# Kernel tuning notes

Measured on AMD Instinct MI355X. Metric: run time of the kernel, lower is better.

## Reference

```python
import jax, jax.numpy as jnp
import numpy as np

N_ATOM, N_CHI, N_BOND, N_DIR = 119, 3, 5, 3
NUM_LAYER, EMB, FEAT, NG = 5, 300, 256, 4096
N_NODES, N_EDGES = 100000, 200000


def setup_inputs() -> dict:
    key = jax.random.key(0)
    ks = jax.random.split(key, 16)
    N, E = N_NODES, N_EDGES
    r = lambda k, s, sc: jax.random.normal(k, s, jnp.float32) * sc
    inp = {}
    inp["atom_type"] = jax.random.randint(ks[0], (N,), 0, N_ATOM, dtype=jnp.int32)
    inp["chirality"] = jax.random.randint(ks[1], (N,), 0, N_CHI, dtype=jnp.int32)
    inp["edge_index"] = jax.random.randint(ks[2], (2, E), 0, N, dtype=jnp.int32)
    inp["edge_type"] = jax.random.randint(ks[3], (E,), 0, 4, dtype=jnp.int32)
    inp["edge_dir"] = jax.random.randint(ks[4], (E,), 0, N_DIR, dtype=jnp.int32)
    inp["batch"] = jnp.sort(jax.random.randint(ks[5], (N,), 0, NG, dtype=jnp.int32))
    inp["atom_emb1"] = r(ks[6], (N_ATOM, EMB), 0.02)
    inp["atom_emb2"] = r(ks[7], (N_CHI, EMB), 0.02)
    inp["W"] = r(ks[8], (NUM_LAYER, EMB, EMB), 0.05)
    inp["b"] = jnp.zeros((NUM_LAYER, EMB), jnp.float32)
    inp["ee1"] = r(ks[9], (NUM_LAYER, N_BOND, 1), 0.5)
    inp["ee2"] = r(ks[10], (NUM_LAYER, N_DIR, 1), 0.5)
    inp["bn_gamma"] = jnp.ones((NUM_LAYER, EMB), jnp.float32)
    inp["bn_beta"] = jnp.zeros((NUM_LAYER, EMB), jnp.float32)
    inp["feat_W"] = r(ks[11], (EMB, FEAT), 0.05)
    inp["feat_b"] = jnp.zeros((FEAT,), jnp.float32)
    inp["head_W1"] = r(ks[12], (FEAT, FEAT // 2), 0.08)
    inp["head_b1"] = jnp.zeros((FEAT // 2,), jnp.float32)
    inp["head_W2"] = r(ks[13], (FEAT // 2, 2), 0.1)
    inp["head_b2"] = jnp.zeros((2,), jnp.float32)
    return inp


def reference(atom_type, chirality, edge_index, edge_type, edge_dir, batch,
              atom_emb1, atom_emb2, W, b, ee1, ee2, bn_gamma, bn_beta,
              feat_W, feat_b, head_W1, head_b1, head_W2, head_b2):
    N = atom_type.shape[0]
    # add self loops (edge_attr: bond_type=4, direction=0)
    loops = jnp.arange(N, dtype=edge_index.dtype)
    row = jnp.concatenate([edge_index[0], loops])
    col = jnp.concatenate([edge_index[1], loops])
    et = jnp.concatenate([edge_type, jnp.full((N,), 4, edge_type.dtype)])
    ed = jnp.concatenate([edge_dir, jnp.zeros((N,), edge_dir.dtype)])

    h = atom_emb1[atom_type] + atom_emb2[chirality]  # [N, EMB]
    for l in range(NUM_LAYER):
        hx = h @ W[l]                                  # [N, EMB]
        edge_emb = ee1[l][et] + ee2[l][ed]             # [E+N, 1]
        msg = hx[row] + edge_emb                       # gather + broadcast add
        out = jax.ops.segment_sum(msg, col, num_segments=N) + b[l]
        # BatchNorm1d (training-mode batch stats, eps=1e-5)
        mean = out.mean(axis=0)
        var = out.var(axis=0)
        h = bn_gamma[l] * (out - mean) * jax.lax.rsqrt(var + 1e-5) + bn_beta[l]
        if l < NUM_LAYER - 1:
            h = jax.nn.relu(h)  # drop_ratio=0 -> dropout is identity

    # global mean pool over graphs
    sums = jax.ops.segment_sum(h, batch, num_segments=NG)              # [NG, EMB]
    counts = jax.ops.segment_sum(jnp.ones((N, 1), h.dtype), batch, num_segments=NG)
    hg = sums / jnp.maximum(counts, 1.0)

    hf = hg @ feat_W + feat_b                                          # [NG, FEAT]
    pred = jax.nn.softplus(hf @ head_W1 + head_b1) @ head_W2 + head_b2  # [NG, 2]
    return hf, pred
```

## Files before the change

### kernel.cpp

```cpp
#include <hip/hip_runtime.h>
#include <math.h>

typedef unsigned short u16;
typedef unsigned int u32;
typedef short v8s __attribute__((ext_vector_type(8)));
typedef float v4f __attribute__((ext_vector_type(4)));

#define EMB 300
#define SP 320
#define NGRP 4096
#define FEAT 256
#define MT 128
#define NT 160
#define NCOMB 357
#define NREP 32

__device__ __forceinline__ u16 f2bf(float x) {
    u32 u = __float_as_uint(x);
    u += 0x7FFFu + ((u >> 16) & 1u);
    return (u16)(u >> 16);
}
__device__ __forceinline__ float bf2f(u16 h) {
    return __uint_as_float((u32)h << 16);
}
__device__ __forceinline__ void unpack8(uint4 w, float* o) {
    const u32* p = &w.x;
#pragma unroll
    for (int q = 0; q < 4; q++) {
        o[2 * q]     = __uint_as_float(p[q] << 16);
        o[2 * q + 1] = __uint_as_float(p[q] & 0xFFFF0000u);
    }
}
__device__ __forceinline__ v8s clampA(uint4 w, float4 ta, float4 tb) {
    const u32* p = &w.x;
    float t[8] = {ta.x, ta.y, ta.z, ta.w, tb.x, tb.y, tb.z, tb.w};
    u32 o[4];
#pragma unroll
    for (int q = 0; q < 4; q++) {
        float lo = __uint_as_float(p[q] << 16);
        float hi = __uint_as_float(p[q] & 0xFFFF0000u);
        lo = fmaxf(lo, t[2 * q]);
        hi = fmaxf(hi, t[2 * q + 1]);
        o[q] = (__float_as_uint(lo) >> 16) | (__float_as_uint(hi) & 0xFFFF0000u);
    }
    uint4 r = make_uint4(o[0], o[1], o[2], o[3]);
    return *(v8s*)&r;
}
__device__ __forceinline__ void dma16(const u16* g, u16* l) {
    __builtin_amdgcn_global_load_lds(
        (const __attribute__((address_space(1))) unsigned int*)g,
        (__attribute__((address_space(3))) unsigned int*)l, 16, 0, 0);
}

__global__ void k_prep_n(const int* __restrict__ at, const int* __restrict__ ch,
                         int* __restrict__ c9, int* __restrict__ deg,
                         int* __restrict__ cursor, int N) {
    int n = blockIdx.x * blockDim.x + threadIdx.x;
    if (n < N) {
        c9[n] = at[n] * 3 + ch[n];
        deg[n] = 0;
        cursor[n] = 0;
    }
}

__global__ void k_count(const int* __restrict__ col, int* __restrict__ deg, int E) {
    int e = blockIdx.x * blockDim.x + threadIdx.x;
    if (e < E) atomicAdd(&deg[col[e]], 1);
}

__global__ __launch_bounds__(256) void k_bsum(const int* __restrict__ deg,
                                              int* __restrict__ bsum, int N) {
    int base = blockIdx.x * 1024 + threadIdx.x * 4;
    int s = 0;
    if (base + 3 < N) {
        int4 v = *(const int4*)(deg + base);
        s = v.x + v.y + v.z + v.w;
    } else {
        for (int j = 0; j < 4; j++) if (base + j < N) s += deg[base + j];
    }
    __shared__ int red[256];
    red[threadIdx.x] = s;
    __syncthreads();
    for (int off = 128; off > 0; off >>= 1) {
        if (threadIdx.x < off) red[threadIdx.x] += red[threadIdx.x + off];
        __syncthreads();
    }
    if (threadIdx.x == 0) bsum[blockIdx.x] = red[0];
}

__global__ __launch_bounds__(128) void k_scanb(const int* __restrict__ bsum,
                                               int* __restrict__ boff, int NB) {
    __shared__ int sh[128];
    int t = threadIdx.x;
    int v = (t < NB) ? bsum[t] : 0;
    sh[t] = v;
    __syncthreads();
    for (int off = 1; off < 128; off <<= 1) {
        int add = (t >= off) ? sh[t - off] : 0;
        __syncthreads();
        sh[t] += add;
        __syncthreads();
    }
    if (t < NB) boff[t] = sh[t] - v;
}

__global__ __launch_bounds__(256) void k_indptr(const int* __restrict__ deg,
                                                const int* __restrict__ boff,
                                                int* __restrict__ indptr, int N) {
    int b = blockIdx.x, t = threadIdx.x;
    int base = b * 1024 + t * 4;
    int v[4] = {0, 0, 0, 0};
    if (base + 3 < N) {
        int4 w = *(const int4*)(deg + base);
        v[0] = w.x; v[1] = w.y; v[2] = w.z; v[3] = w.w;
    } else {
        for (int j = 0; j < 4; j++) if (base + j < N) v[j] = deg[base + j];
    }
    int tsum = v[0] + v[1] + v[2] + v[3];
    __shared__ int sh[256];
    sh[t] = tsum;
    __syncthreads();
    for (int off = 1; off < 256; off <<= 1) {
        int add = (t >= off) ? sh[t - off] : 0;
        __syncthreads();
        sh[t] += add;
        __syncthreads();
    }
    int run = boff[b] + sh[t] - tsum;
    for (int j = 0; j < 4; j++) {
        run += v[j];
        if (base + j < N) indptr[base + j + 1] = run;
    }
    if (b == 0 && t == 0) indptr[0] = 0;
}

__global__ void k_fill(const int* __restrict__ row, const int* __restrict__ col,
                       const int* __restrict__ et, const int* __restrict__ ed,
                       const int* __restrict__ indptr, int* __restrict__ cursor,
                       int* __restrict__ packed, int E) {
    int e = blockIdx.x * blockDim.x + threadIdx.x;
    if (e >= E) return;
    int c = col[e];
    int pos = indptr[c] + atomicAdd(&cursor[c], 1);
    packed[pos] = row[e] | ((et[e] * 3 + ed[e]) << 17);
}

__global__ void k_comb(const float* __restrict__ e1, const float* __restrict__ e2,
                       u16* __restrict__ comb) {
    int idx = blockIdx.x * blockDim.x + threadIdx.x;
    if (idx >= NCOMB * 40) return;
    int row = idx / 40, f = idx % 40;
    int at = row / 3, ch = row % 3;
    u32 o[4];
#pragma unroll
    for (int q = 0; q < 4; q++) {
        int c0 = f * 8 + q * 2;
        float x0 = 0.f, x1 = 0.f;
        if (c0 < EMB)     x0 = e1[(size_t)at * EMB + c0] + e2[(size_t)ch * EMB + c0];
        if (c0 + 1 < EMB) x1 = e1[(size_t)at * EMB + c0 + 1] + e2[(size_t)ch * EMB + c0 + 1];
        o[q] = (u32)f2bf(x0) | ((u32)f2bf(x1) << 16);
    }
    *(uint4*)(comb + (size_t)row * SP + f * 8) = make_uint4(o[0], o[1], o[2], o[3]);
}

__global__ __launch_bounds__(320) void k_wprep(
    const float* __restrict__ Wl, const float* __restrict__ sc,
    const float* __restrict__ sh, u16* __restrict__ Wt, float* __restrict__ srow) {
    __shared__ float wred[5];
    int n = blockIdx.x;
    int k = threadIdx.x;
    float w = 0.f;
    if (n < EMB && k < EMB) w = Wl[(size_t)k * EMB + n];
    Wt[(size_t)n * SP + k] = f2bf(w * sc[k]);
    float s = (k < EMB) ? sh[k] * w : 0.f;
#pragma unroll
    for (int o2 = 32; o2 > 0; o2 >>= 1) s += __shfl_down(s, o2);
    if ((k & 63) == 0) wred[k >> 6] = s;
    __syncthreads();
    if (k == 0) {
        float t = wred[0] + wred[1] + wred[2] + wred[3] + wred[4];
        srow[n] = (n < EMB) ? t : 0.f;
    }
}

__global__ void k_ident(float* __restrict__ sc, float* __restrict__ sh,
                        float* __restrict__ thr, float* __restrict__ colstats) {
    int c = threadIdx.x;
    if (c < SP) {
        sc[c] = (c < EMB) ? 1.f : 0.f;
        sh[c] = 0.f;
        thr[c] = -__builtin_inff();
        for (int r = 0; r < NREP; r++) {
            colstats[r * 2 * SP + c] = 0.f;
            colstats[r * 2 * SP + SP + c] = 0.f;
        }
    }
}

__global__ void k_finalize(float* __restrict__ cs,
                           const float* __restrict__ gamma, const float* __restrict__ beta,
                           float* __restrict__ sc, float* __restrict__ sh,
                           float* __restrict__ thr, int N) {
    int c = threadIdx.x;
    if (c >= SP) return;
    float s1 = 0.f, s2 = 0.f;
    for (int r = 0; r < NREP; r++) {
        s1 += cs[r * 2 * SP + c];
        s2 += cs[r * 2 * SP + SP + c];
        cs[r * 2 * SP + c] = 0.f;
        cs[r * 2 * SP + SP + c] = 0.f;
    }
    if (c < EMB) {
        float inv = 1.f / (float)N;
        float mean = s1 * inv;
        float var = s2 * inv - mean * mean;
        float rstd = rsqrtf(fmaxf(var, 0.f) + 1e-5f);
        float s = gamma[c] * rstd;
        float b = beta[c] - mean * s;
        sc[c] = s;
        sh[c] = b;
        thr[c] = bf2f(f2bf(-b / s));
    } else {
        sc[c] = 0.f; sh[c] = 0.f; thr[c] = -__builtin_inff();
    }
}

__global__ __launch_bounds__(256) void k_gemm(
    const u16* __restrict__ A, const u16* __restrict__ Wt,
    const float* __restrict__ thr, const float* __restrict__ srow,
    u16* __restrict__ C, int M, const int* __restrict__ rowmap) {
    __shared__ __align__(16) u16 sm[21504];

    int m0 = blockIdx.y * MT;
    int n0 = blockIdx.x * NT;
    int tid = threadIdx.x;
    int wave = tid >> 6, lane = tid & 63;
    int wm = wave >> 1, wn = wave & 1;
    int lm = lane & 15, quad = lane >> 4;

    int ar0 = min(m0 + (tid >> 2), M - 1);
    int ar1 = min(m0 + 64 + (tid >> 2), M - 1);
    if (rowmap) { ar0 = rowmap[ar0]; ar1 = rowmap[ar1]; }
    const u16* ag0 = A + (size_t)ar0 * SP + (tid & 3) * 8;
    const u16* ag1 = A + (size_t)ar1 * SP + (tid & 3) * 8;
    const u16* bg0 = Wt + (size_t)(n0 + (tid >> 2)) * SP + (tid & 3) * 8;
    const u16* bg1 = Wt + (size_t)(n0 + 64 + (tid >> 2)) * SP + (tid & 3) * 8;
    const u16* bg2 = Wt + (size_t)(n0 + 128 + (tid >> 2)) * SP + (tid & 3) * 8;

    const float* tp = thr + quad * 8;

    v4f acc[4][5];
#pragma unroll
    for (int nf = 0; nf < 5; nf++) {
        float sv = srow[n0 + wn * 80 + nf * 16 + lm];
#pragma unroll
        for (int mf = 0; mf < 4; mf++)
            acc[mf][nf] = (v4f){sv, sv, sv, sv};
    }

    auto issue = [&](int d, int kt) {
        int ko = kt * 32;
        u16* ad = sm + d * 4096;
        u16* bd = sm + 8192 + d * 5120;
        dma16(ag0 + ko, ad + tid * 8);
        dma16(ag1 + ko, ad + (256 + tid) * 8);
        dma16(bg0 + ko, bd + tid * 8);
        dma16(bg1 + ko, bd + (256 + tid) * 8);
        if (tid < 128) dma16(bg2 + ko, bd + (512 + tid) * 8);
    };

    issue(0, 0);
    for (int kt = 0; kt < SP / 32; kt++) {
        __syncthreads();
        if (kt + 1 < SP / 32) issue((kt + 1) & 1, kt + 1);
        const u16* as = sm + (kt & 1) * 4096;
        const u16* bs = sm + 8192 + (kt & 1) * 5120;
        float4 ta = *(const float4*)(tp + kt * 32);
        float4 tb = *(const float4*)(tp + kt * 32 + 4);
        v8s b[5], a[4];
#pragma unroll
        for (int nf = 0; nf < 5; nf++)
            b[nf] = *(const v8s*)(bs + (wn * 80 + nf * 16 + lm) * 32 + quad * 8);
#pragma unroll
        for (int mf = 0; mf < 4; mf++) {
            uint4 w = *(const uint4*)(as + (wm * 64 + mf * 16 + lm) * 32 + quad * 8);
            a[mf] = clampA(w, ta, tb);
        }
#pragma unroll
        for (int nf = 0; nf < 5; nf++)
#pragma unroll
            for (int mf = 0; mf < 4; mf++)
                acc[mf][nf] = __builtin_amdgcn_mfma_f32_16x16x32_bf16(a[mf], b[nf], acc[mf][nf], 0, 0, 0);
    }

    __syncthreads();
#pragma unroll
    for (int mf = 0; mf < 4; mf++)
#pragma unroll
        for (int nf = 0; nf < 5; nf++)
#pragma unroll
            for (int r = 0; r < 4; r++)
                sm[(wm * 64 + mf * 16 + quad * 4 + r) * 168 + wn * 80 + nf * 16 + lm] =
                    f2bf(acc[mf][nf][r]);
    __syncthreads();
#pragma unroll
    for (int i = 0; i < 10; i++) {
        int slot = tid + i * 256;
        int r = slot / 20, cg = slot % 20;
        if (m0 + r < M)
            *(uint4*)(C + (size_t)(m0 + r) * SP + n0 + cg * 8) =
                *(const uint4*)(sm + r * 168 + cg * 8);
    }
}

__global__ __launch_bounds__(320) void k_aggf(
    const u16* __restrict__ Q, const int* __restrict__ indptr,
    const int* __restrict__ packed, const float* __restrict__ e1,
    const float* __restrict__ e2, u16* __restrict__ P,
    float* __restrict__ colstats, int N) {
    __shared__ float tab[15];
    __shared__ float part[8][328];
    int tid = threadIdx.x;
    if (tid < 15) tab[tid] = e1[tid / 3] + e2[tid % 3];
    __syncthreads();
    int f = tid % 40;
    int slot = tid / 40;
    int n = blockIdx.x * 8 + slot;

    float psum[8] = {0, 0, 0, 0, 0, 0, 0, 0};
    float psq[8]  = {0, 0, 0, 0, 0, 0, 0, 0};

    if (n < N) {
        float acc[8];
        unpack8(*(const uint4*)(Q + (size_t)n * SP + f * 8), acc);
        float s = tab[12];
        int i = indptr[n], e = indptr[n + 1];
        int pk = (i < e) ? packed[i] : 0;
        while (i < e) {
            uint4 g = *(const uint4*)(Q + (size_t)(pk & 0x1FFFF) * SP + f * 8);
            int nx = i + 1;
            int pkn = (nx < e) ? packed[nx] : 0;
            float t[8];
            unpack8(g, t);
#pragma unroll
            for (int q = 0; q < 8; q++) acc[q] += t[q];
            s += tab[pk >> 17];
            i = nx; pk = pkn;
        }
        u32 o[4];
#pragma unroll
        for (int q = 0; q < 4; q++) {
            float r0 = acc[2 * q] + s;
            float r1 = acc[2 * q + 1] + s;
            psum[2 * q] = r0;      psum[2 * q + 1] = r1;
            psq[2 * q]  = r0 * r0; psq[2 * q + 1]  = r1 * r1;
            o[q] = (u32)f2bf(r0) | ((u32)f2bf(r1) << 16);
        }
        *(uint4*)(P + (size_t)n * SP + f * 8) = make_uint4(o[0], o[1], o[2], o[3]);
    }

    int rep = (blockIdx.x & (NREP - 1)) * 2 * SP;
#pragma unroll
    for (int j = 0; j < 8; j++) part[slot][f * 8 + j] = psum[j];
    __syncthreads();
    {
        float s = 0.f;
#pragma unroll
        for (int k = 0; k < 8; k++) s += part[k][tid];
        atomicAdd(&colstats[rep + tid], s);
    }
    __syncthreads();
#pragma unroll
    for (int j = 0; j < 8; j++) part[slot][f * 8 + j] = psq[j];
    __syncthreads();
    {
        float s = 0.f;
#pragma unroll
        for (int k = 0; k < 8; k++) s += part[k][tid];
        atomicAdd(&colstats[rep + SP + tid], s);
    }
}

__global__ void k_bounds(const int* __restrict__ batch, int* __restrict__ gstart, int N) {
    int n = blockIdx.x * blockDim.x + threadIdx.x;
    if (n > N) return;
    int bcur = (n < N) ? batch[n] : NGRP;
    int bprev = (n > 0) ? batch[n - 1] : -1;
    for (int g = bprev + 1; g <= bcur; g++) gstart[g] = n;
}

__global__ __launch_bounds__(320) void k_pool(
    const u16* __restrict__ P, const float* __restrict__ sc,
    const float* __restrict__ sh, const int* __restrict__ gstart,
    float* __restrict__ hg) {
    int tid = threadIdx.x;
    int g = blockIdx.x * 8 + tid / 40;
    int f = tid % 40;
    int r0 = gstart[g], r1 = gstart[g + 1];
    int cnt = r1 - r0;
    float acc[8] = {0, 0, 0, 0, 0, 0, 0, 0};
    for (int r = r0; r < r1; r++) {
        float t[8];
        unpack8(*(const uint4*)(P + (size_t)r * SP + f * 8), t);
#pragma unroll
        for (int j = 0; j < 8; j++) acc[j] += t[j];
    }
    float inv = 1.f / (float)max(cnt, 1);
#pragma unroll
    for (int j = 0; j < 8; j++) {
        int c = f * 8 + j;
        if (c < EMB)
            hg[(size_t)g * EMB + c] = (acc[j] * sc[c] + (float)cnt * sh[c]) * inv;
    }
}

__global__ __launch_bounds__(256) void k_feat(const float* __restrict__ hg,
                                              const float* __restrict__ fW,
                                              const float* __restrict__ fb,
                                              float* __restrict__ hf) {
    __shared__ float hgs[16 * EMB];
    int g0 = blockIdx.x * 16;
    int tid = threadIdx.x;
    for (int i = tid; i < 16 * EMB; i += 256) {
        int gi = i / EMB, c = i % EMB;
        hgs[i] = hg[(size_t)(g0 + gi) * EMB + c];
    }
    __syncthreads();
    float acc[16];
    float fbv = fb[tid];
#pragma unroll
    for (int gi = 0; gi < 16; gi++) acc[gi] = fbv;
    for (int k = 0; k < EMB; k++) {
        float w = fW[(size_t)k * FEAT + tid];
#pragma unroll
        for (int gi = 0; gi < 16; gi++) acc[gi] += hgs[gi * EMB + k] * w;
    }
#pragma unroll
    for (int gi = 0; gi < 16; gi++) hf[(size_t)(g0 + gi) * FEAT + tid] = acc[gi];
}

__global__ __launch_bounds__(128) void k_head(const float* __restrict__ hf,
                                              const float* __restrict__ W1,
                                              const float* __restrict__ b1,
                                              const float* __restrict__ W2,
                                              const float* __restrict__ b2,
                                              float* __restrict__ pred) {
    __shared__ float hfs[8 * FEAT];
    __shared__ float sred[2][8][2];
    int g0 = blockIdx.x * 8;
    int tid = threadIdx.x;
    for (int i = tid; i < 8 * FEAT; i += 128) {
        int gi = i >> 8, k = i & 255;
        hfs[i] = hf[(size_t)(g0 + gi) * FEAT + k];
    }
    __syncthreads();
    float acc[8];
    float b1v = b1[tid];
#pragma unroll
    for (int gi = 0; gi < 8; gi++) acc[gi] = b1v;
    for (int k = 0; k < FEAT; k++) {
        float w = W1[(size_t)k * 128 + tid];
#pragma unroll
        for (int gi = 0; gi < 8; gi++) acc[gi] += hfs[gi * FEAT + k] * w;
    }
    float w20 = W2[tid * 2], w21 = W2[tid * 2 + 1];
    int wv = tid >> 6;
#pragma unroll
    for (int gi = 0; gi < 8; gi++) {
        float x = acc[gi];
        float t = fmaxf(x, 0.f) + log1pf(expf(-fabsf(x)));
        float p0 = t * w20, p1 = t * w21;
#pragma unroll
        for (int off = 32; off > 0; off >>= 1) {
            p0 += __shfl_down(p0, off);
            p1 += __shfl_down(p1, off);
        }
        if ((tid & 63) == 0) { sred[wv][gi][0] = p0; sred[wv][gi][1] = p1; }
    }
    __syncthreads();
    if (tid < 16) {
        int gi = tid >> 1, o = tid & 1;
        pred[(size_t)(g0 + gi) * 2 + o] = sred[0][gi][o] + sred[1][gi][o] + b2[o];
    }
}

extern "C" void kernel_launch(void* const* d_in, const int* in_sizes, int n_in,
                              void* d_out, int out_size, void* d_ws, size_t ws_size,
                              hipStream_t stream) {
    const int* atom_type = (const int*)d_in[0];
    const int* chir      = (const int*)d_in[1];
    const int* eidx      = (const int*)d_in[2];
    const int* etype     = (const int*)d_in[3];
    const int* edir      = (const int*)d_in[4];
    const int* batch     = (const int*)d_in[5];
    const float* emb1    = (const float*)d_in[6];
    const float* emb2    = (const float*)d_in[7];
    const float* W       = (const float*)d_in[8];
    const float* ee1     = (const float*)d_in[10];
    const float* ee2     = (const float*)d_in[11];
    const float* gamma   = (const float*)d_in[12];
    const float* beta    = (const float*)d_in[13];
    const float* featW   = (const float*)d_in[14];
    const float* featb   = (const float*)d_in[15];
    const float* hW1     = (const float*)d_in[16];
    const float* hb1     = (const float*)d_in[17];
    const float* hW2     = (const float*)d_in[18];
    const float* hb2     = (const float*)d_in[19];

    int N = in_sizes[0];
    int E = in_sizes[2] / 2;
    const int* erow = eidx;
    const int* ecol = eidx + E;

    size_t off = 0;
    char* base = (char*)d_ws;
    auto carve = [&](size_t bytes) -> void* {
        void* p = base + off;
        off += (bytes + 255) & ~(size_t)255;
        return p;
    };
    u16*   P        = (u16*)  carve((size_t)N * SP * 2);
    u16*   Q        = (u16*)  carve((size_t)N * SP * 2);
    u16*   Wt       = (u16*)  carve((size_t)SP * SP * 2);
    u16*   comb     = (u16*)  carve((size_t)NCOMB * SP * 2);
    int*   c9map    = (int*)  carve((size_t)N * 4);
    int*   deg      = (int*)  carve((size_t)N * 4);
    int*   cursor   = (int*)  carve((size_t)N * 4);
    int*   indptr   = (int*)  carve((size_t)(N + 1) * 4);
    int*   packed   = (int*)  carve((size_t)E * 4);
    int*   bsum     = (int*)  carve(1024 * 4);
    int*   boff     = (int*)  carve(1024 * 4);
    float* colstats = (float*)carve((size_t)NREP * 2 * SP * 4);
    float* scale_id = (float*)carve(SP * 4);
    float* shift_id = (float*)carve(SP * 4);
    float* thr_id   = (float*)carve(SP * 4);
    float* scale_bn = (float*)carve(SP * 4);
    float* shift_bn = (float*)carve(SP * 4);
    float* thr_bn   = (float*)carve(SP * 4);
    float* srow     = (float*)carve(SP * 4);
    int*   gstart   = (int*)  carve((size_t)(NGRP + 1) * 4);
    float* hg       = (float*)carve((size_t)NGRP * EMB * 4);

    float* hf   = (float*)d_out;
    float* pred = (float*)d_out + (size_t)NGRP * FEAT;

    int eb = (E + 255) / 256;
    int NB = (N + 1023) / 1024;
    k_prep_n<<<(N + 255) / 256, 256, 0, stream>>>(atom_type, chir, c9map, deg, cursor, N);
    k_count<<<eb, 256, 0, stream>>>(ecol, deg, E);
    k_bsum<<<NB, 256, 0, stream>>>(deg, bsum, N);
    k_scanb<<<1, 128, 0, stream>>>(bsum, boff, NB);
    k_indptr<<<NB, 256, 0, stream>>>(deg, boff, indptr, N);
    k_fill<<<eb, 256, 0, stream>>>(erow, ecol, etype, edir, indptr, cursor, packed, E);

    k_comb<<<(NCOMB * 40 + 255) / 256, 256, 0, stream>>>(emb1, emb2, comb);
    k_ident<<<1, SP, 0, stream>>>(scale_id, shift_id, thr_id, colstats);

    const float* sc = scale_id;
    const float* sh = shift_id;
    const float* th = thr_id;
    dim3 ggrid(2, (N + MT - 1) / MT);
    int ab = (N + 7) / 8;
    for (int l = 0; l < 5; l++) {
        k_wprep<<<SP, 320, 0, stream>>>(W + (size_t)l * EMB * EMB, sc, sh, Wt, srow);
        if (l == 0)
            k_gemm<<<ggrid, 256, 0, stream>>>(comb, Wt, th, srow, Q, N, c9map);
        else
            k_gemm<<<ggrid, 256, 0, stream>>>(P, Wt, th, srow, Q, N, nullptr);
        k_aggf<<<ab, 320, 0, stream>>>(Q, indptr, packed, ee1 + l * 5, ee2 + l * 3, P,
                                       colstats, N);
        k_finalize<<<1, SP, 0, stream>>>(colstats, gamma + l * EMB, beta + l * EMB,
                                         scale_bn, shift_bn, thr_bn, N);
        sc = scale_bn; sh = shift_bn; th = thr_bn;
    }

    k_bounds<<<(N + 1 + 255) / 256, 256, 0, stream>>>(batch, gstart, N);
    k_pool<<<NGRP / 8, 320, 0, stream>>>(P, scale_bn, shift_bn, gstart, hg);
    k_feat<<<NGRP / 16, 256, 0, stream>>>(hg, featW, featb, hf);
    k_head<<<NGRP / 8, 128, 0, stream>>>(hf, hW1, hb1, hW2, hb2, pred);
}
```

Measured before the change: 718.9 us.

## Load GEMM B operand directly from global and halve shared memory footprint

The GEMM kernel stops staging the weight (B) tiles through LDS and has each lane read its B fragment straight from global memory, relying on cache since the weights are small and reused across blocks. The epilogue writes the output tile through LDS in two halves so the shared buffer can shrink to half its former size. The intent is to cut LDS traffic and footprint so more blocks can be resident per CU. In exchange, B reads become per-lane global loads with 16-byte strided access inside the inner loop, which adds latency and an extra barrier in the epilogue.

```diff
diff --git a/kernel.cpp b/kernel.cpp
--- a/kernel.cpp
+++ b/kernel.cpp
@@ -229,7 +229,7 @@
     const u16* __restrict__ A, const u16* __restrict__ Wt,
     const float* __restrict__ thr, const float* __restrict__ srow,
     u16* __restrict__ C, int M, const int* __restrict__ rowmap) {
-    __shared__ __align__(16) u16 sm[21504];
+    __shared__ __align__(16) u16 sm[10752];
 
     int m0 = blockIdx.y * MT;
     int n0 = blockIdx.x * NT;
@@ -243,9 +243,7 @@
     if (rowmap) { ar0 = rowmap[ar0]; ar1 = rowmap[ar1]; }
     const u16* ag0 = A + (size_t)ar0 * SP + (tid & 3) * 8;
     const u16* ag1 = A + (size_t)ar1 * SP + (tid & 3) * 8;
-    const u16* bg0 = Wt + (size_t)(n0 + (tid >> 2)) * SP + (tid & 3) * 8;
-    const u16* bg1 = Wt + (size_t)(n0 + 64 + (tid >> 2)) * SP + (tid & 3) * 8;
-    const u16* bg2 = Wt + (size_t)(n0 + 128 + (tid >> 2)) * SP + (tid & 3) * 8;
+    const u16* bp = Wt + (size_t)(n0 + wn * 80 + lm) * SP + quad * 8;
 
     const float* tp = thr + quad * 8;
 
@@ -261,12 +259,8 @@
     auto issue = [&](int d, int kt) {
         int ko = kt * 32;
         u16* ad = sm + d * 4096;
-        u16* bd = sm + 8192 + d * 5120;
         dma16(ag0 + ko, ad + tid * 8);
         dma16(ag1 + ko, ad + (256 + tid) * 8);
-        dma16(bg0 + ko, bd + tid * 8);
-        dma16(bg1 + ko, bd + (256 + tid) * 8);
-        if (tid < 128) dma16(bg2 + ko, bd + (512 + tid) * 8);
     };
 
     issue(0, 0);
@@ -274,13 +268,12 @@
         __syncthreads();
         if (kt + 1 < SP / 32) issue((kt + 1) & 1, kt + 1);
         const u16* as = sm + (kt & 1) * 4096;
-        const u16* bs = sm + 8192 + (kt & 1) * 5120;
         float4 ta = *(const float4*)(tp + kt * 32);
         float4 tb = *(const float4*)(tp + kt * 32 + 4);
         v8s b[5], a[4];
 #pragma unroll
         for (int nf = 0; nf < 5; nf++)
-            b[nf] = *(const v8s*)(bs + (wn * 80 + nf * 16 + lm) * 32 + quad * 8);
+            b[nf] = *(const v8s*)(bp + (size_t)nf * 16 * SP + kt * 32);
 #pragma unroll
         for (int mf = 0; mf < 4; mf++) {
             uint4 w = *(const uint4*)(as + (wm * 64 + mf * 16 + lm) * 32 + quad * 8);
@@ -295,21 +288,28 @@
 
     __syncthreads();
 #pragma unroll
-    for (int mf = 0; mf < 4; mf++)
-#pragma unroll
-        for (int nf = 0; nf < 5; nf++)
-#pragma unroll
-            for (int r = 0; r < 4; r++)
-                sm[(wm * 64 + mf * 16 + quad * 4 + r) * 168 + wn * 80 + nf * 16 + lm] =
-                    f2bf(acc[mf][nf][r]);
-    __syncthreads();
-#pragma unroll
-    for (int i = 0; i < 10; i++) {
-        int slot = tid + i * 256;
-        int r = slot / 20, cg = slot % 20;
-        if (m0 + r < M)
-            *(uint4*)(C + (size_t)(m0 + r) * SP + n0 + cg * 8) =
-                *(const uint4*)(sm + r * 168 + cg * 8);
+    for (int p = 0; p < 2; p++) {
+#pragma unroll
+        for (int mf2 = 0; mf2 < 2; mf2++) {
+            int mf = p * 2 + mf2;
+#pragma unroll
+            for (int nf = 0; nf < 5; nf++)
+#pragma unroll
+                for (int r = 0; r < 4; r++)
+                    sm[(wm * 32 + mf2 * 16 + quad * 4 + r) * 168 + wn * 80 + nf * 16 + lm] =
+                        f2bf(acc[mf][nf][r]);
+        }
+        __syncthreads();
+#pragma unroll
+        for (int i = 0; i < 5; i++) {
+            int slot = tid + i * 256;
+            int lr = slot / 20, cg = slot % 20;
+            int grow = m0 + (lr >> 5) * 64 + p * 32 + (lr & 31);
+            if (grow < M)
+                *(uint4*)(C + (size_t)grow * SP + n0 + cg * 8) =
+                    *(const uint4*)(sm + lr * 168 + cg * 8);
+        }
+        __syncthreads();
     }
 }
 
```

After: 819.6 us. +14.0%, slower.
